# Performance work log

Measured on AMD Instinct MI355X. Metric: run time of the kernel, lower is better.

## Reference

```python
import jax, jax.numpy as jnp
import numpy as np

IN, E, T = 1024, 512, 4096

def _lstm_dir(xs, Wih, Whh, b):
    # xs: [T, E]; Wih: [4E, E]; Whh: [4E, E]; b: [4E] (b_ih + b_hh)
    H = Whh.shape[1]
    def step(carry, xt):
        h, c = carry
        g = xt @ Wih.T + h @ Whh.T + b  # [4E], torch gate order: i, f, g, o
        i, f, gg, o = jnp.split(g, 4)
        i = jax.nn.sigmoid(i); f = jax.nn.sigmoid(f)
        gg = jnp.tanh(gg); o = jax.nn.sigmoid(o)
        c = f * c + i * gg
        h = o * jnp.tanh(c)
        return (h, c), h
    init = (jnp.zeros((H,), xs.dtype), jnp.zeros((H,), xs.dtype))
    _, hs = jax.lax.scan(step, init, xs)
    return hs  # [T, H]

def setup_inputs() -> dict:
    key = jax.random.key(0)
    ks = jax.random.split(key, 12)
    inp = {
        "x": jax.random.normal(ks[0], (1, T, IN), jnp.float32),
        "A": jax.random.normal(ks[1], (IN, E), jnp.float32) * 0.02,
        "B": jax.random.normal(ks[2], (IN, E), jnp.float32) * 0.02,
        "U": jax.random.normal(ks[3], (IN, E), jnp.float32) * 0.02,
        "w_ih_f": jax.random.normal(ks[4], (4 * E, E), jnp.float32) * 0.05,
        "w_hh_f": jax.random.normal(ks[5], (4 * E, E), jnp.float32) * 0.05,
        "b_ih_f": jax.random.normal(ks[6], (4 * E,), jnp.float32) * 0.05,
        "b_hh_f": jnp.zeros((4 * E,), jnp.float32),
        "w_ih_b": jax.random.normal(ks[7], (4 * E, E), jnp.float32) * 0.05,
        "w_hh_b": jax.random.normal(ks[8], (4 * E, E), jnp.float32) * 0.05,
        "b_ih_b": jax.random.normal(ks[9], (4 * E,), jnp.float32) * 0.05,
        "b_hh_b": jnp.zeros((4 * E,), jnp.float32),
        "final_w": jax.random.normal(ks[10], (1, 2 * E), jnp.float32) * 0.05,
        "final_b": jnp.zeros((1,), jnp.float32),
    }
    return inp

def reference(x, A, B, U, w_ih_f, w_hh_f, b_ih_f, b_hh_f,
              w_ih_b, w_hh_b, b_ih_b, b_hh_b, final_w, final_b):
    a = jnp.einsum('bti,ie->bte', x, A)  # [1,T,E]
    b = jnp.einsum('bti,ie->bte', x, B)
    u = jnp.einsum('bti,ie->bte', x, U)
    scores = jnp.einsum('bqe,bke->bqk', u, a)      # unscaled attention [1,T,T]
    p = jax.nn.softmax(scores, axis=-1)
    out_vec = jnp.einsum('bqk,bke->bqe', p, b)     # [1,T,E]
    u_mod = (u * out_vec)[0]                       # gate, batch=1 -> [T,E]
    hf = _lstm_dir(u_mod, w_ih_f, w_hh_f, b_ih_f + b_hh_f)
    hb = _lstm_dir(u_mod[::-1], w_ih_b, w_hh_b, b_ih_b + b_hh_b)[::-1]
    otp = jnp.concatenate([hf, hb], axis=-1)[None]  # [1,T,2E]
    score = jnp.einsum('bte,oe->bto', otp, final_w) + final_b  # [1,T,1]
    return score
```

## Files before the change

kernel.cpp:

```cpp
#include <hip/hip_runtime.h>
#include <cstddef>
#include <cstdint>

#define T_   4096
#define IN_  1024
#define E_   512
#define G4_  2048

typedef unsigned short ushort_t;
typedef __attribute__((ext_vector_type(8))) short bf16x8;
typedef __attribute__((ext_vector_type(4))) float f32x4;

__device__ __forceinline__ ushort_t rne_bf16(float x) {
    unsigned int u = __float_as_uint(x);
    return (ushort_t)((u + 0x7FFFu + ((u >> 16) & 1u)) >> 16);
}
__device__ __forceinline__ float bf2f(ushort_t h) {
    return __uint_as_float((unsigned int)h << 16);
}

__global__ __launch_bounds__(256) void mfma_gemm(
    const ushort_t* __restrict__ Ah, const ushort_t* __restrict__ Al,
    const ushort_t* __restrict__ Bh, const ushort_t* __restrict__ Bl,
    float* __restrict__ Cf, ushort_t* __restrict__ Ch, ushort_t* __restrict__ Cl,
    int M, int N, int K, int nA,
    const float* __restrict__ bias1, const float* __restrict__ bias2)
{
    __shared__ ushort_t sAh[128 * 40], sAl[128 * 40];
    __shared__ ushort_t sBh[128 * 40], sBl[128 * 40];

    const int tid  = threadIdx.x;
    const int wv   = tid >> 6;
    const int lane = tid & 63;
    const int quad = lane >> 4;
    const int l16  = lane & 15;
    const int bm = blockIdx.y * 128, bn = blockIdx.x * 128;
    const int wrow = (wv & 1) * 64, wcol = (wv >> 1) * 64;

    f32x4 acc[4][4];
#pragma unroll
    for (int i = 0; i < 4; ++i)
#pragma unroll
        for (int j = 0; j < 4; ++j) acc[i][j] = (f32x4){0.f, 0.f, 0.f, 0.f};

    const int r0 = tid >> 2;
    const int ks = (tid & 3) * 8;

    for (int k0 = 0; k0 < K; k0 += 32) {
        const size_t ga0 = (size_t)(bm + r0) * K + k0 + ks;
        const size_t ga1 = (size_t)(bm + r0 + 64) * K + k0 + ks;
        const size_t gb0 = (size_t)(bn + r0) * K + k0 + ks;
        const size_t gb1 = (size_t)(bn + r0 + 64) * K + k0 + ks;
        uint4 vA0 = *(const uint4*)(Ah + ga0);
        uint4 vA1 = *(const uint4*)(Ah + ga1);
        uint4 vB0h = *(const uint4*)(Bh + gb0);
        uint4 vB1h = *(const uint4*)(Bh + gb1);
        uint4 vB0l = *(const uint4*)(Bl + gb0);
        uint4 vB1l = *(const uint4*)(Bl + gb1);
        uint4 vA0l, vA1l;
        if (nA == 2) { vA0l = *(const uint4*)(Al + ga0); vA1l = *(const uint4*)(Al + ga1); }
        __syncthreads();
        *(uint4*)&sAh[r0 * 40 + ks] = vA0;
        *(uint4*)&sAh[(r0 + 64) * 40 + ks] = vA1;
        *(uint4*)&sBh[r0 * 40 + ks] = vB0h;
        *(uint4*)&sBh[(r0 + 64) * 40 + ks] = vB1h;
        *(uint4*)&sBl[r0 * 40 + ks] = vB0l;
        *(uint4*)&sBl[(r0 + 64) * 40 + ks] = vB1l;
        if (nA == 2) {
            *(uint4*)&sAl[r0 * 40 + ks] = vA0l;
            *(uint4*)&sAl[(r0 + 64) * 40 + ks] = vA1l;
        }
        __syncthreads();

        bf16x8 afh[4], afl[4], bfh[4], bfl[4];
#pragma unroll
        for (int f = 0; f < 4; ++f) {
            const int ar = (wrow + f * 16 + l16) * 40 + quad * 8;
            const int br = (wcol + f * 16 + l16) * 40 + quad * 8;
            afh[f] = *(const bf16x8*)&sAh[ar];
            bfh[f] = *(const bf16x8*)&sBh[br];
            bfl[f] = *(const bf16x8*)&sBl[br];
            if (nA == 2) afl[f] = *(const bf16x8*)&sAl[ar];
        }
#pragma unroll
        for (int fi = 0; fi < 4; ++fi)
#pragma unroll
            for (int fj = 0; fj < 4; ++fj) {
                acc[fi][fj] = __builtin_amdgcn_mfma_f32_16x16x32_bf16(
                    afh[fi], bfh[fj], acc[fi][fj], 0, 0, 0);
                acc[fi][fj] = __builtin_amdgcn_mfma_f32_16x16x32_bf16(
                    afh[fi], bfl[fj], acc[fi][fj], 0, 0, 0);
                if (nA == 2)
                    acc[fi][fj] = __builtin_amdgcn_mfma_f32_16x16x32_bf16(
                        afl[fi], bfh[fj], acc[fi][fj], 0, 0, 0);
            }
    }

#pragma unroll
    for (int fi = 0; fi < 4; ++fi)
#pragma unroll
        for (int fj = 0; fj < 4; ++fj) {
            const int col = bn + wcol + fj * 16 + l16;
            float bv = 0.f;
            if (bias1) bv += bias1[col];
            if (bias2) bv += bias2[col];
#pragma unroll
            for (int r = 0; r < 4; ++r) {
                const int row = bm + wrow + fi * 16 + quad * 4 + r;
                const float v = acc[fi][fj][r] + bv;
                const size_t o = (size_t)row * N + col;
                if (Cf) Cf[o] = v;
                if (Ch) {
                    const ushort_t h = rne_bf16(v);
                    Ch[o] = h;
                    if (Cl) Cl[o] = rne_bf16(v - bf2f(h));
                }
            }
        }
}

__global__ __launch_bounds__(256) void conv_hl(
    const float* __restrict__ in, ushort_t* __restrict__ oh, ushort_t* __restrict__ ol)
{
    const size_t i = ((size_t)blockIdx.x * 256 + threadIdx.x) * 4;
    float4 v = *(const float4*)(in + i);
    ushort4 h, l;
    h.x = rne_bf16(v.x); l.x = rne_bf16(v.x - bf2f(h.x));
    h.y = rne_bf16(v.y); l.y = rne_bf16(v.y - bf2f(h.y));
    h.z = rne_bf16(v.z); l.z = rne_bf16(v.z - bf2f(h.z));
    h.w = rne_bf16(v.w); l.w = rne_bf16(v.w - bf2f(h.w));
    *(ushort4*)(oh + i) = h;
    *(ushort4*)(ol + i) = l;
}

__global__ __launch_bounds__(256) void conv_hl_T(
    const float* __restrict__ in, ushort_t* __restrict__ oh, ushort_t* __restrict__ ol,
    int R, int C)
{
    __shared__ float t[32][33];
    const int tx = threadIdx.x & 31, ty = threadIdx.x >> 5;
    const int gr = blockIdx.y * 32, gc = blockIdx.x * 32;
#pragma unroll
    for (int i = 0; i < 4; ++i)
        t[ty + 8 * i][tx] = in[(size_t)(gr + ty + 8 * i) * C + gc + tx];
    __syncthreads();
#pragma unroll
    for (int i = 0; i < 4; ++i) {
        const int oc = gc + ty + 8 * i;
        const float v = t[tx][ty + 8 * i];
        const ushort_t h = rne_bf16(v);
        oh[(size_t)oc * R + gr + tx] = h;
        ol[(size_t)oc * R + gr + tx] = rne_bf16(v - bf2f(h));
    }
}

__global__ __launch_bounds__(256) void softmax_kernel(
    const float* __restrict__ S, ushort_t* __restrict__ P)
{
    __shared__ float red[8];
    const float* p = S + (size_t)blockIdx.x * T_;
    ushort_t* pr = P + (size_t)blockIdx.x * T_;
    const int tid = threadIdx.x;
    const int wid = tid >> 6;
    const int lane = tid & 63;
    float4 v[4];
#pragma unroll
    for (int i = 0; i < 4; ++i) v[i] = ((const float4*)p)[tid + 256 * i];
    float m = -3.0e38f;
#pragma unroll
    for (int i = 0; i < 4; ++i)
        m = fmaxf(m, fmaxf(fmaxf(v[i].x, v[i].y), fmaxf(v[i].z, v[i].w)));
#pragma unroll
    for (int o = 32; o; o >>= 1) m = fmaxf(m, __shfl_xor(m, o));
    if (lane == 0) red[wid] = m;
    __syncthreads();
    m = fmaxf(fmaxf(red[0], red[1]), fmaxf(red[2], red[3]));
    float s = 0.f;
#pragma unroll
    for (int i = 0; i < 4; ++i) {
        v[i].x = __expf(v[i].x - m); v[i].y = __expf(v[i].y - m);
        v[i].z = __expf(v[i].z - m); v[i].w = __expf(v[i].w - m);
        s += v[i].x + v[i].y + v[i].z + v[i].w;
    }
#pragma unroll
    for (int o = 32; o; o >>= 1) s += __shfl_xor(s, o);
    if (lane == 0) red[4 + wid] = s;
    __syncthreads();
    s = red[4] + red[5] + red[6] + red[7];
    const float inv = 1.f / s;
#pragma unroll
    for (int i = 0; i < 4; ++i) {
        ushort4 o4;
        o4.x = rne_bf16(v[i].x * inv); o4.y = rne_bf16(v[i].y * inv);
        o4.z = rne_bf16(v[i].z * inv); o4.w = rne_bf16(v[i].w * inv);
        ((ushort4*)pr)[tid + 256 * i] = o4;
    }
}

__global__ __launch_bounds__(256) void umod_kernel(
    const ushort_t* __restrict__ uh, const ushort_t* __restrict__ ul,
    const float* __restrict__ ov,
    ushort_t* __restrict__ mh, ushort_t* __restrict__ ml)
{
    const size_t i = ((size_t)blockIdx.x * 256 + threadIdx.x) * 4;
    ushort4 h4 = *(const ushort4*)(uh + i);
    ushort4 l4 = *(const ushort4*)(ul + i);
    float4 o = *(const float4*)(ov + i);
    float4 m;
    m.x = (bf2f(h4.x) + bf2f(l4.x)) * o.x;
    m.y = (bf2f(h4.y) + bf2f(l4.y)) * o.y;
    m.z = (bf2f(h4.z) + bf2f(l4.z)) * o.z;
    m.w = (bf2f(h4.w) + bf2f(l4.w)) * o.w;
    ushort4 oh, ol;
    oh.x = rne_bf16(m.x); ol.x = rne_bf16(m.x - bf2f(oh.x));
    oh.y = rne_bf16(m.y); ol.y = rne_bf16(m.y - bf2f(oh.y));
    oh.z = rne_bf16(m.z); ol.z = rne_bf16(m.z - bf2f(oh.z));
    oh.w = rne_bf16(m.w); ol.w = rne_bf16(m.w - bf2f(oh.w));
    *(ushort4*)(mh + i) = oh;
    *(ushort4*)(ml + i) = ol;
}

#define NU_ 16
#define PACE_TICKS 25L

__global__ __launch_bounds__(256, 1) void lstm_kernel(
    const float* __restrict__ whh_f, const float* __restrict__ whh_b,
    const ushort_t* __restrict__ xg_f, const ushort_t* __restrict__ xg_b,
    float* __restrict__ hf_out, float* __restrict__ hb_out,
    unsigned int* __restrict__ hbuf)
{
    __shared__ float sh[2][4 * 132];

    const int tid  = threadIdx.x;
    const int dir  = blockIdx.x >> 5;
    const int w    = blockIdx.x & 31;
    const int lane = tid & 63;
    const int j    = tid >> 4;
    const int g    = (tid >> 2) & 3;
    const int c    = tid & 3;
    const int lu   = lane >> 4;
    const int u0   = w * NU_;

    const float* whh = dir ? whh_b : whh_f;
    const ushort_t* xg = dir ? xg_b : xg_f;
    float* hout = dir ? hb_out : hf_out;
    unsigned int* hb = hbuf + dir * 1024;

    float wreg[128];
    {
        const float* wr = whh + (size_t)(g * E_ + u0 + j) * E_ + 128 * c;
#pragma unroll
        for (int i = 0; i < 32; ++i)
            *(float4*)&wreg[4 * i] = *(const float4*)(wr + 4 * i);
    }
    for (int i = tid; i < 2 * 4 * 132; i += 256) ((float*)sh)[i] = 0.f;

    float creg = 0.f;
    const float gsc  = (g == 2) ? 2.f : 1.f;
    const float gmul = (g == 2) ? 2.f : 1.f;
    const float gadd = (g == 2) ? -1.f : 0.f;

    float xv = bf2f(xg[(size_t)(dir ? (T_ - 1) : 0) * G4_ + g * E_ + u0 + j]);
    unsigned int budget = 1u << 23;

    const int e0 = 2 * tid;
    const int p0 = (e0 >> 7) * 132 + (e0 & 127);

    long long tpub = (long long)__builtin_amdgcn_s_memrealtime();

    for (int s = 0; s < T_; ++s) {
        const int t = dir ? (T_ - 1 - s) : s;

        if (s > 0) {
            while ((long long)__builtin_amdgcn_s_memrealtime() - tpub < PACE_TICKS) {}
            const unsigned int tt = (unsigned int)(s - 1) & 0xFFFFu;
            const unsigned long long* src =
                (const unsigned long long*)(hb + ((s - 1) & 1) * 512);
            unsigned long long v;
            for (;;) {
                v = __hip_atomic_load(src + tid, __ATOMIC_RELAXED,
                                      __HIP_MEMORY_SCOPE_AGENT);
                const unsigned int lo = (unsigned int)v;
                const unsigned int hi = (unsigned int)(v >> 32);
                if (((lo >> 16) == tt && (hi >> 16) == tt) || !--budget) break;
            }
            float2 hv;
            hv.x = __uint_as_float((unsigned int)v << 16);
            hv.y = __uint_as_float((unsigned int)(v >> 32) << 16);
            *(float2*)&sh[s & 1][p0] = hv;
        }
        __syncthreads();

        const float* hc = &sh[s & 1][132 * c];
        float sx = 0.f, sy = 0.f, sz = 0.f, sw = 0.f;
#pragma unroll
        for (int i = 0; i < 32; ++i) {
            const float4 h4 = *(const float4*)&hc[4 * i];
            sx = fmaf(wreg[4 * i + 0], h4.x, sx);
            sy = fmaf(wreg[4 * i + 1], h4.y, sy);
            sz = fmaf(wreg[4 * i + 2], h4.z, sz);
            sw = fmaf(wreg[4 * i + 3], h4.w, sw);
        }
        float sum = (sx + sy) + (sz + sw);
        sum += __shfl_xor(sum, 1);
        sum += __shfl_xor(sum, 2);

        const float xx = (sum + xv) * gsc;
        const float rr = __builtin_amdgcn_rcpf(1.f + __expf(-xx));
        const float val = fmaf(rr, gmul, gadd);

        const int base = 16 * lu + c;
        const float iv = __shfl(val, base);
        const float fv = __shfl(val, base + 4);
        const float gv = __shfl(val, base + 8);
        const float ov = __shfl(val, base + 12);
        creg = fmaf(fv, creg, iv * gv);
        const float th = fmaf(2.f, __builtin_amdgcn_rcpf(1.f + __expf(-2.f * creg)), -1.f);
        const float h = ov * th;

        if ((tid & 15) == 0) {
            const unsigned int ub = __float_as_uint(h);
            const unsigned int b16 = (ub + 0x7FFFu + ((ub >> 16) & 1u)) >> 16;
            const unsigned int pkt = (((unsigned int)s & 0xFFFFu) << 16) | b16;
            __hip_atomic_store(hb + (s & 1) * 512 + u0 + j, pkt,
                               __ATOMIC_RELAXED, __HIP_MEMORY_SCOPE_AGENT);
            hout[(size_t)t * E_ + u0 + j] = h;
        }
        tpub = (long long)__builtin_amdgcn_s_memrealtime();

        if (s + 1 < T_)
            xv = bf2f(xg[(size_t)(dir ? (T_ - 2 - s) : (s + 1)) * G4_ + g * E_ + u0 + j]);
    }
}

__global__ __launch_bounds__(256) void final_kernel(
    const float* __restrict__ hf, const float* __restrict__ hb,
    const float* __restrict__ fw, const float* __restrict__ fb,
    float* __restrict__ out)
{
    const int t = blockIdx.x * 4 + (threadIdx.x >> 6);
    const int lane = threadIdx.x & 63;
    float s = 0.f;
#pragma unroll
    for (int i = 0; i < 8; ++i) {
        const int e = lane + 64 * i;
        s += hf[(size_t)t * E_ + e] * fw[e];
    }
#pragma unroll
    for (int i = 0; i < 8; ++i) {
        const int e = lane + 64 * i;
        s += hb[(size_t)t * E_ + e] * fw[E_ + e];
    }
#pragma unroll
    for (int o = 32; o; o >>= 1) s += __shfl_xor(s, o);
    if (lane == 0) out[t] = s + fb[0];
}

extern "C" void kernel_launch(void* const* d_in, const int* in_sizes, int n_in,
                              void* d_out, int out_size, void* d_ws, size_t ws_size,
                              hipStream_t stream)
{
    const float* x     = (const float*)d_in[0];
    const float* Amat  = (const float*)d_in[1];
    const float* Bmat  = (const float*)d_in[2];
    const float* Umat  = (const float*)d_in[3];
    const float* wih_f = (const float*)d_in[4];
    const float* whh_f = (const float*)d_in[5];
    const float* bih_f = (const float*)d_in[6];
    const float* bhh_f = (const float*)d_in[7];
    const float* wih_b = (const float*)d_in[8];
    const float* whh_b = (const float*)d_in[9];
    const float* bih_b = (const float*)d_in[10];
    const float* bhh_b = (const float*)d_in[11];
    const float* fw    = (const float*)d_in[12];
    const float* fb    = (const float*)d_in[13];
    float* out = (float*)d_out;
    char* wsb = (char*)d_ws;
    const size_t MB = 1048576ull;

    ushort_t* uh  = (ushort_t*)(wsb + 0 * MB);
    ushort_t* ul  = (ushort_t*)(wsb + 4 * MB);
    float*    bfp = (float*)   (wsb + 8 * MB);
    ushort_t* xh  = (ushort_t*)(wsb + 16 * MB);
    ushort_t* xl  = (ushort_t*)(wsb + 24 * MB);
    ushort_t* ATh = (ushort_t*)(wsb + 32 * MB);
    ushort_t* ATl = (ushort_t*)(wsb + 33 * MB);
    ushort_t* BTh = (ushort_t*)(wsb + 34 * MB);
    ushort_t* BTl = (ushort_t*)(wsb + 35 * MB);
    ushort_t* UTh = (ushort_t*)(wsb + 36 * MB);
    ushort_t* UTl = (ushort_t*)(wsb + 37 * MB);
    ushort_t* ah  = (ushort_t*)(wsb + 38 * MB);
    ushort_t* al  = (ushort_t*)(wsb + 42 * MB);
    ushort_t* bTh = (ushort_t*)(wsb + 46 * MB);
    ushort_t* bTl = (ushort_t*)(wsb + 50 * MB);
    float*    S_  = (float*)   (wsb + 56 * MB);
    ushort_t* Ph  = (ushort_t*)(wsb + 8 * MB);
    float*    ov_ = (float*)   (wsb + 56 * MB);
    ushort_t* umh = (ushort_t*)(wsb + 64 * MB);
    ushort_t* uml = (ushort_t*)(wsb + 68 * MB);
    ushort_t* wfh = (ushort_t*)(wsb + 72 * MB);
    ushort_t* wfl = (ushort_t*)(wsb + 74 * MB);
    ushort_t* wbh = (ushort_t*)(wsb + 76 * MB);
    ushort_t* wbl = (ushort_t*)(wsb + 78 * MB);
    ushort_t* xfg = (ushort_t*)(wsb + 80 * MB);
    ushort_t* xbg = (ushort_t*)(wsb + 96 * MB);
    float*    hf_ = (float*)   (wsb + 0 * MB);
    float*    hb_ = (float*)   (wsb + 8 * MB);
    unsigned int* hbuf_ = (unsigned int*)(wsb + 112 * MB);

    dim3 blk(256);

    conv_hl<<<dim3(4096), blk, 0, stream>>>(x, xh, xl);
    conv_hl_T<<<dim3(16, 32), blk, 0, stream>>>(Amat, ATh, ATl, 1024, 512);
    conv_hl_T<<<dim3(16, 32), blk, 0, stream>>>(Bmat, BTh, BTl, 1024, 512);
    conv_hl_T<<<dim3(16, 32), blk, 0, stream>>>(Umat, UTh, UTl, 1024, 512);
    mfma_gemm<<<dim3(4, 32), blk, 0, stream>>>(xh, xl, ATh, ATl, nullptr, ah, al,
                                               T_, E_, IN_, 2, nullptr, nullptr);
    mfma_gemm<<<dim3(4, 32), blk, 0, stream>>>(xh, xl, BTh, BTl, bfp, nullptr, nullptr,
                                               T_, E_, IN_, 2, nullptr, nullptr);
    mfma_gemm<<<dim3(4, 32), blk, 0, stream>>>(xh, xl, UTh, UTl, nullptr, uh, ul,
                                               T_, E_, IN_, 2, nullptr, nullptr);
    mfma_gemm<<<dim3(32, 32), blk, 0, stream>>>(uh, ul, ah, al, S_, nullptr, nullptr,
                                                T_, T_, E_, 2, nullptr, nullptr);
    conv_hl_T<<<dim3(16, 128), blk, 0, stream>>>(bfp, bTh, bTl, 4096, 512);
    softmax_kernel<<<dim3(T_), blk, 0, stream>>>(S_, Ph);
    mfma_gemm<<<dim3(4, 32), blk, 0, stream>>>(Ph, nullptr, bTh, bTl, ov_, nullptr, nullptr,
                                               T_, E_, T_, 1, nullptr, nullptr);
    umod_kernel<<<dim3(2048), blk, 0, stream>>>(uh, ul, ov_, umh, uml);
    conv_hl<<<dim3(1024), blk, 0, stream>>>(wih_f, wfh, wfl);
    conv_hl<<<dim3(1024), blk, 0, stream>>>(wih_b, wbh, wbl);
    mfma_gemm<<<dim3(16, 32), blk, 0, stream>>>(umh, uml, wfh, wfl, nullptr, xfg, nullptr,
                                                T_, G4_, E_, 2, bih_f, bhh_f);
    mfma_gemm<<<dim3(16, 32), blk, 0, stream>>>(umh, uml, wbh, wbl, nullptr, xbg, nullptr,
                                                T_, G4_, E_, 2, bih_b, bhh_b);
    lstm_kernel<<<dim3(64), blk, 0, stream>>>(whh_f, whh_b, xfg, xbg, hf_, hb_, hbuf_);
    final_kernel<<<dim3(1024), blk, 0, stream>>>(hf_, hb_, fw, fb, out);
}
```

Measured before the change: 7.556 ms.

## Pin LSTM direction blocks to one XCD and exchange hidden state via local L2

Launches 256 blocks and keeps only those with blockIdx%8 in {0,1}, relying on round-robin XCD assignment so each direction's 32 blocks share one XCD's L2. Hidden-state packets are also written to a second buffer and polled with sc0 L2-level loads, with a shorter pacing delay, to cut cross-block handoff latency on the serial recurrence. If the local copy is not seen after a few spins it falls back to agent-scope loads, and after repeated fallbacks it reverts to the old path. It depends on undocumented block-to-XCD placement and on workgroup-scope stores becoming visible in shared L2.

```diff
diff --git a/kernel.cpp b/kernel.cpp
--- a/kernel.cpp
+++ b/kernel.cpp
@@ -17,6 +17,13 @@
 }
 __device__ __forceinline__ float bf2f(ushort_t h) {
     return __uint_as_float((unsigned int)h << 16);
+}
+
+__device__ __forceinline__ unsigned long long load_l2_u64(const unsigned long long* p) {
+    unsigned long long v;
+    asm volatile("global_load_dwordx2 %0, %1, off sc0\n\ts_waitcnt vmcnt(0)"
+                 : "=v"(v) : "v"(p) : "memory");
+    return v;
 }
 
 __global__ __launch_bounds__(256) void mfma_gemm(
@@ -221,19 +228,24 @@
 }
 
 #define NU_ 16
-#define PACE_TICKS 25L
+#define PACE_L 8L
+#define PACE_A 25L
 
 __global__ __launch_bounds__(256, 1) void lstm_kernel(
     const float* __restrict__ whh_f, const float* __restrict__ whh_b,
     const ushort_t* __restrict__ xg_f, const ushort_t* __restrict__ xg_b,
     float* __restrict__ hf_out, float* __restrict__ hb_out,
-    unsigned int* __restrict__ hbuf)
-{
+    unsigned int* __restrict__ hbuf,
+    unsigned int* __restrict__ lbuf)
+{
+    const int xcd = blockIdx.x & 7;
+    if (xcd >= 2) return;
+    const int dir = xcd;
+    const int w   = blockIdx.x >> 3;
+
     __shared__ float sh[2][4 * 132];
 
     const int tid  = threadIdx.x;
-    const int dir  = blockIdx.x >> 5;
-    const int w    = blockIdx.x & 31;
     const int lane = tid & 63;
     const int j    = tid >> 4;
     const int g    = (tid >> 2) & 3;
@@ -245,6 +257,7 @@
     const ushort_t* xg = dir ? xg_b : xg_f;
     float* hout = dir ? hb_out : hf_out;
     unsigned int* hb = hbuf + dir * 1024;
+    unsigned int* lb = lbuf + dir * 1024;
 
     float wreg[128];
     {
@@ -267,22 +280,44 @@
     const int p0 = (e0 >> 7) * 132 + (e0 & 127);
 
     long long tpub = (long long)__builtin_amdgcn_s_memrealtime();
+    int use_local = 1, failcnt = 0;
 
     for (int s = 0; s < T_; ++s) {
         const int t = dir ? (T_ - 1 - s) : s;
 
         if (s > 0) {
-            while ((long long)__builtin_amdgcn_s_memrealtime() - tpub < PACE_TICKS) {}
+            const long long pt = use_local ? PACE_L : PACE_A;
+            while ((long long)__builtin_amdgcn_s_memrealtime() - tpub < pt) {}
             const unsigned int tt = (unsigned int)(s - 1) & 0xFFFFu;
-            const unsigned long long* src =
+            const unsigned long long* srcL =
+                (const unsigned long long*)(lb + ((s - 1) & 1) * 512);
+            const unsigned long long* srcA =
                 (const unsigned long long*)(hb + ((s - 1) & 1) * 512);
             unsigned long long v;
-            for (;;) {
-                v = __hip_atomic_load(src + tid, __ATOMIC_RELAXED,
-                                      __HIP_MEMORY_SCOPE_AGENT);
-                const unsigned int lo = (unsigned int)v;
-                const unsigned int hi = (unsigned int)(v >> 32);
-                if (((lo >> 16) == tt && (hi >> 16) == tt) || !--budget) break;
+            if (use_local) {
+                bool fell = false;
+                int spins = 0;
+                for (;;) {
+                    v = load_l2_u64(srcL + tid);
+                    if (((unsigned int)v >> 16) == tt &&
+                        ((unsigned int)(v >> 32) >> 16) == tt) break;
+                    if (++spins >= 6) {
+                        v = __hip_atomic_load(srcA + tid, __ATOMIC_RELAXED,
+                                              __HIP_MEMORY_SCOPE_AGENT);
+                        if (((unsigned int)v >> 16) == tt &&
+                            ((unsigned int)(v >> 32) >> 16) == tt) { fell = true; break; }
+                        if (!--budget) break;
+                    }
+                }
+                if (__ballot(fell)) { if (++failcnt >= 8) use_local = 0; }
+                else failcnt = 0;
+            } else {
+                for (;;) {
+                    v = __hip_atomic_load(srcA + tid, __ATOMIC_RELAXED,
+                                          __HIP_MEMORY_SCOPE_AGENT);
+                    if ((((unsigned int)v >> 16) == tt &&
+                         ((unsigned int)(v >> 32) >> 16) == tt) || !--budget) break;
+                }
             }
             float2 hv;
             hv.x = __uint_as_float((unsigned int)v << 16);
@@ -322,6 +357,8 @@
             const unsigned int ub = __float_as_uint(h);
             const unsigned int b16 = (ub + 0x7FFFu + ((ub >> 16) & 1u)) >> 16;
             const unsigned int pkt = (((unsigned int)s & 0xFFFFu) << 16) | b16;
+            __hip_atomic_store(lb + (s & 1) * 512 + u0 + j, pkt,
+                               __ATOMIC_RELAXED, __HIP_MEMORY_SCOPE_WORKGROUP);
             __hip_atomic_store(hb + (s & 1) * 512 + u0 + j, pkt,
                                __ATOMIC_RELAXED, __HIP_MEMORY_SCOPE_AGENT);
             hout[(size_t)t * E_ + u0 + j] = h;
@@ -407,6 +444,7 @@
     float*    hf_ = (float*)   (wsb + 0 * MB);
     float*    hb_ = (float*)   (wsb + 8 * MB);
     unsigned int* hbuf_ = (unsigned int*)(wsb + 112 * MB);
+    unsigned int* lbuf_ = (unsigned int*)(wsb + 113 * MB);
 
     dim3 blk(256);
 
@@ -433,6 +471,7 @@
                                                 T_, G4_, E_, 2, bih_f, bhh_f);
     mfma_gemm<<<dim3(16, 32), blk, 0, stream>>>(umh, uml, wbh, wbl, nullptr, xbg, nullptr,
                                                 T_, G4_, E_, 2, bih_b, bhh_b);
-    lstm_kernel<<<dim3(64), blk, 0, stream>>>(whh_f, whh_b, xfg, xbg, hf_, hb_, hbuf_);
+    lstm_kernel<<<dim3(256), blk, 0, stream>>>(whh_f, whh_b, xfg, xbg, hf_, hb_,
+                                               hbuf_, lbuf_);
     final_kernel<<<dim3(1024), blk, 0, stream>>>(hf_, hb_, fw, fb, out);
 }
```

Measured after the change: 6.739 ms. 10.8% less time.
